# Kernel tuning notes

Hardware: AMD Instinct MI355X
Metric: run time of the kernel (lower is better)

## Reference

```python
import jax, jax.numpy as jnp
import numpy as np

B, LAT, HID = 256, 20, 128
G, BIN = 25000, 25       # original_dim, bin_size
C = 7                    # max_cp + 1 copy-number states
GB = G // BIN            # rho head output dim


def setup_inputs() -> dict:
    key = jax.random.key(0)
    ks = jax.random.split(key, 16)
    s = 0.01  # TruncatedNormal(stddev=0.01) init
    return {
        "z": jax.random.normal(ks[0], (B, LAT), jnp.float32),
        "w0": jax.random.normal(ks[1], (LAT, HID), jnp.float32) * s,
        "b0": jnp.zeros((HID,), jnp.float32),
        "g0": jnp.ones((HID,), jnp.float32),
        "be0": jnp.zeros((HID,), jnp.float32),
        "m0": jax.random.normal(ks[2], (HID,), jnp.float32) * 0.1,
        "v0": jax.random.uniform(ks[3], (HID,), jnp.float32, 0.5, 1.5),
        "w1": jax.random.normal(ks[4], (HID, HID), jnp.float32) * s,
        "b1": jnp.zeros((HID,), jnp.float32),
        "g1": jnp.ones((HID,), jnp.float32),
        "be1": jnp.zeros((HID,), jnp.float32),
        "m1": jax.random.normal(ks[5], (HID,), jnp.float32) * 0.1,
        "v1": jax.random.uniform(ks[6], (HID,), jnp.float32, 0.5, 1.5),
        "wr": jax.random.normal(ks[7], (HID, G), jnp.float32) * s,
        "br": jnp.zeros((G,), jnp.float32),
        "wd": jax.random.normal(ks[8], (HID, G), jnp.float32) * s,
        "bd": jnp.zeros((G,), jnp.float32),
        "wrho": jax.random.normal(ks[9], (C, HID, GB), jnp.float32) * s,
        "brho": jnp.zeros((C, GB), jnp.float32),
        "ws": jax.random.normal(ks[10], (G,), jnp.float32) * 0.05,
        "bs": jax.random.normal(ks[11], (G,), jnp.float32) * 0.05,
    }


def reference(z, w0, b0, g0, be0, m0, v0, w1, b1, g1, be1, m1, v1,
              wr, br, wd, bd, wrho, brho, ws, bs):
    BN_EPS = 1e-3
    EPS = 1e-20
    TEMP = 0.1

    def bn(x, gamma, beta, mean, var):
        # inference-mode BatchNormalization(momentum=0.01, epsilon=0.001)
        return (x - mean) * jax.lax.rsqrt(var + BN_EPS) * gamma + beta

    # FullyConnLayer x2: Dense -> BN -> ReLU
    x = jax.nn.relu(bn(z @ w0 + b0, g0, be0, m0, v0))
    x = jax.nn.relu(bn(x @ w1 + b1, g1, be1, m1, v1))

    theta = jnp.exp(x @ wr + br)        # [B, G]
    pi_drop = x @ wd + bd               # [B, G]

    # max_cp+1 rho Dense heads fused into a single batched GEMM -> [C, B, GB]
    rho = jnp.einsum('bh,cho->cbo', x, wrho) + brho[:, None, :]
    rho = jax.nn.softmax(rho, axis=0)   # softmax over copy-number states

    # GumbelSoftmaxSampling: stack(axis=1) -> [B, C, GB]
    rho_b = jnp.transpose(rho, (1, 0, 2))
    gene_rho = jnp.repeat(rho_b, BIN, axis=-1)        # [B, C, G]
    pi = jnp.transpose(gene_rho, (0, 2, 1))           # [B, G, C]

    u = jax.random.uniform(jax.random.key(42), pi.shape, jnp.float32)
    gnoise = -jnp.log(-jnp.log(u + EPS) + EPS)
    y = jax.nn.softmax((jnp.log(pi + EPS) + gnoise) / TEMP, axis=-1)
    y_hard = (y == jnp.max(y, axis=-1, keepdims=True)).astype(jnp.float32)
    y = jax.lax.stop_gradient(y_hard - y) + y         # straight-through

    # multiply by copy-number index matrix and reduce -> expected/sampled copy
    cvals = jnp.arange(C, dtype=jnp.float32)
    sample = jnp.sum(y * cvals, axis=-1)              # [B, G]

    # ScaleLayer: sigmoid(x * w + b)
    mu = jax.nn.sigmoid(sample * ws + bs)             # [B, G]
    return (mu, theta, pi_drop, sample, pi)
```

## Files before the change

### kernel.cpp

```cpp
#include <hip/hip_runtime.h>

#define B 256
#define LAT 20
#define HID 128
#define G 25000
#define GB 1000
#define NC 7

typedef __attribute__((ext_vector_type(8))) short short8;
typedef __attribute__((ext_vector_type(4))) float f32x4;

__device__ __forceinline__ unsigned short f2bf(float f) {
  unsigned int u = __float_as_uint(f);
  u += 0x7fffu + ((u >> 16) & 1u);
  return (unsigned short)(u >> 16);
}

__device__ __forceinline__ unsigned int threefry_xor(unsigned int idx) {
  unsigned int x0 = 0u;
  unsigned int x1 = idx + 42u;
#define TF_R(r) { x0 += x1; x1 = (x1 << r) | (x1 >> (32 - r)); x1 ^= x0; }
  TF_R(13) TF_R(15) TF_R(26) TF_R(6)
  x0 += 42u;          x1 += 0x1BD11BF1u;
  TF_R(17) TF_R(29) TF_R(16) TF_R(24)
  x0 += 0x1BD11BF0u;  x1 += 2u;
  TF_R(13) TF_R(15) TF_R(26) TF_R(6)
   x1 += 45u;
  TF_R(17) TF_R(29) TF_R(16) TF_R(24)
  x0 += 42u;          x1 += 0x1BD11BF4u;
  TF_R(13) TF_R(15) TF_R(26) TF_R(6)
  x0 += 0x1BD11BF0u;  x1 += 5u;
#undef TF_R
  return x0 ^ x1;
}

__global__ void k_mlp(const float* __restrict__ z,  const float* __restrict__ w0,
                      const float* __restrict__ b0, const float* __restrict__ g0,
                      const float* __restrict__ be0, const float* __restrict__ m0,
                      const float* __restrict__ v0,
                      const float* __restrict__ w1, const float* __restrict__ b1,
                      const float* __restrict__ g1, const float* __restrict__ be1,
                      const float* __restrict__ m1, const float* __restrict__ v1,
                      double* __restrict__ x64, unsigned short* __restrict__ x_bf) {
  __shared__ double xs[HID];
  const int b = blockIdx.x, h = threadIdx.x;
  double acc = (double)b0[h];
  for (int k = 0; k < LAT; ++k)
    acc += (double)z[b * LAT + k] * (double)w0[k * HID + h];
  double y = (acc - (double)m0[h]) * (1.0 / sqrt((double)v0[h] + 1e-3)) * (double)g0[h]
             + (double)be0[h];
  y = y > 0.0 ? y : 0.0;
  xs[h] = y;
  __syncthreads();
  double a1 = (double)b1[h];
  for (int k = 0; k < HID; ++k)
    a1 += xs[k] * (double)w1[k * HID + h];
  double y1 = (a1 - (double)m1[h]) * (1.0 / sqrt((double)v1[h] + 1e-3)) * (double)g1[h]
              + (double)be1[h];
  y1 = y1 > 0.0 ? y1 : 0.0;
  x64[h * B + b] = y1;
  x_bf[b * HID + h] = f2bf((float)y1);
}

__global__ void k_trans(const float* __restrict__ wr, const float* __restrict__ wd,
                        unsigned short* __restrict__ wrT, unsigned short* __restrict__ wdT) {
  __shared__ float t[64][65];
  const float* src = blockIdx.z ? wd : wr;
  unsigned short* dst = blockIdx.z ? wdT : wrT;
  const int g0 = blockIdx.x * 64, h0 = blockIdx.y * 64;
#pragma unroll
  for (int i = 0; i < 16; ++i) {
    int f = i * 256 + threadIdx.x;
    int hl = f >> 6, gl = f & 63;
    int g = g0 + gl;
    t[hl][gl] = (g < G) ? src[(h0 + hl) * G + g] : 0.f;
  }
  __syncthreads();
#pragma unroll
  for (int i = 0; i < 16; ++i) {
    int f = i * 256 + threadIdx.x;
    int gl = f >> 6, hl = f & 63;
    int g = g0 + gl;
    if (g < G) dst[(size_t)g * HID + h0 + hl] = f2bf(t[hl][gl]);
  }
}

__global__ __launch_bounds__(256) void k_rho(const double* __restrict__ x64,
                      const float* __restrict__ wrho, const float* __restrict__ brho,
                      float* __restrict__ pi32, float* __restrict__ lp32,
                      double* __restrict__ lp64) {
  __shared__ float wl[NC * HID * 4];
  const int o0 = blockIdx.x * 4, bB = blockIdx.y * 64;
  for (int i = threadIdx.x; i < NC * HID * 4; i += 256) {
    int ol = i & 3, rest = i >> 2;
    int c = rest >> 7, h = rest & 127;
    wl[i] = wrho[(c * HID + h) * GB + o0 + ol];
  }
  __syncthreads();
  const int lane = threadIdx.x & 63, ol = threadIdx.x >> 6;
  const int b = bB + lane, o = o0 + ol;
  double acc[NC];
#pragma unroll
  for (int c = 0; c < NC; ++c) acc[c] = (double)brho[c * GB + o];
  for (int h = 0; h < HID; ++h) {
    double xv = x64[h * B + b];
#pragma unroll
    for (int c = 0; c < NC; ++c)
      acc[c] += xv * (double)wl[(c * HID + h) * 4 + ol];
  }
  double m = acc[0];
#pragma unroll
  for (int c = 1; c < NC; ++c) m = fmax(m, acc[c]);
  double e[NC], s = 0.0;
#pragma unroll
  for (int c = 0; c < NC; ++c) { e[c] = exp(acc[c] - m); s += e[c]; }
  const size_t base = (size_t)o * (NC * B) + b;
#pragma unroll
  for (int c = 0; c < NC; ++c) {
    double pi = e[c] / s;
    double lp = log(pi + 1e-20);
    pi32[base + c * B] = (float)pi;
    lp32[base + c * B] = (float)lp;
    lp64[base + c * B] = lp;
  }
}

__global__ __launch_bounds__(256) void k_main(
    const unsigned short* __restrict__ x_bf,
    const unsigned short* __restrict__ wrT, const unsigned short* __restrict__ wdT,
    const float* __restrict__ br, const float* __restrict__ bd,
    const float* __restrict__ wsc, const float* __restrict__ bsc,
    const float* __restrict__ pi32, const float* __restrict__ lp32,
    const double* __restrict__ lp64, float* __restrict__ out) {
  const int tid = threadIdx.x;
  const int wv = tid >> 6, lane = tid & 63;
  const int n = lane & 15, quad = lane >> 4;
  const int gt = wv & 1;
  const int btbase = blockIdx.y * 8 + (wv >> 1) * 4;
  const int g = blockIdx.x * 32 + gt * 16 + n;
  const bool gvalid = g < G;
  const int gcl = gvalid ? g : G - 1;
  const float brv = br[gcl], bdv = bd[gcl], wsv = wsc[gcl], bsv = bsc[gcl];
  const int o = gcl / 25;
  const float*  lpb = lp32 + (size_t)o * (NC * B);
  const float*  pib = pi32 + (size_t)o * (NC * B);
  const double* lqb = lp64 + (size_t)o * (NC * B);

  short8 fr[4], fd[4];
  {
    const short8* p1 = (const short8*)(wrT + (size_t)gcl * HID + quad * 8);
    const short8* p2 = (const short8*)(wdT + (size_t)gcl * HID + quad * 8);
#pragma unroll
    for (int ks = 0; ks < 4; ++ks) { fr[ks] = p1[ks * 4]; fd[ks] = p2[ks * 4]; }
  }

  for (int bti = 0; bti < 4; ++bti) {
    const int bt = btbase + bti;
    const short8* xp = (const short8*)(x_bf + (size_t)(bt * 16 + n) * HID + quad * 8);
    f32x4 accr = {0.f, 0.f, 0.f, 0.f}, accd = {0.f, 0.f, 0.f, 0.f};
#pragma unroll
    for (int ks = 0; ks < 4; ++ks) {
      short8 fa = xp[ks * 4];
      accr = __builtin_amdgcn_mfma_f32_16x16x32_bf16(fa, fr[ks], accr, 0, 0, 0);
      accd = __builtin_amdgcn_mfma_f32_16x16x32_bf16(fa, fd[ks], accd, 0, 0, 0);
    }
#pragma unroll
    for (int i = 0; i < 4; ++i) {
      const int b = bt * 16 + quad * 4 + i;
      const float th = expf(accr[i] + brv);
      const float pd = accd[i] + bdv;
      float lpv[NC];
#pragma unroll
      for (int c = 0; c < NC; ++c) lpv[c] = lpb[c * B + b];
      unsigned int bits[NC];
      const unsigned int idx0 = (unsigned int)b * 175000u + (unsigned int)g * 7u;
      float best = -3.4e38f, sec = -3.4e38f; int arg = 0;
#pragma unroll
      for (int c = 0; c < NC; ++c) {
        unsigned int bb = threefry_xor(idx0 + (unsigned int)c);
        bits[c] = bb;
        float uf = __uint_as_float((bb >> 9) | 0x3f800000u) - 1.0f;
        float l1 = -logf(uf + 1e-20f);
        float gn = -__logf(l1 + 1e-20f);
        float mv = lpv[c] + gn;
        if (mv > best) { sec = best; best = mv; arg = c; }
        else if (mv > sec) sec = mv;
      }
      int s = arg;
      if (best - sec < 2e-3f) {
        double lv[NC], bestd = -1e300;
#pragma unroll
        for (int c = 0; c < NC; ++c) {
          float uf = __uint_as_float((bits[c] >> 9) | 0x3f800000u) - 1.0f;
          double gn = -log(-log((double)uf + 1e-20) + 1e-20);
          lv[c] = lqb[c * B + b] + gn;
          bestd = fmax(bestd, lv[c]);
        }
        s = 0;
#pragma unroll
        for (int c = 0; c < NC; ++c) if (lv[c] == bestd) s += c;
      }
      if (gvalid) {
        const float smp = (float)s;
        const float mu = 1.f / (1.f + expf(-(smp * wsv + bsv)));
        const size_t og = (size_t)b * G + g;
        out[og] = mu;
        out[6400000 + og] = th;
        out[12800000 + og] = pd;
        out[19200000 + og] = smp;
        const size_t pbo = 25600000 + og * 7;
#pragma unroll
        for (int c = 0; c < NC; ++c) out[pbo + c] = pib[c * B + b];
      }
    }
  }
}

extern "C" void kernel_launch(void* const* d_in, const int* in_sizes, int n_in,
                              void* d_out, int out_size, void* d_ws, size_t ws_size,
                              hipStream_t stream) {
  const float* z   = (const float*)d_in[0];
  const float* w0  = (const float*)d_in[1];
  const float* b0  = (const float*)d_in[2];
  const float* g0  = (const float*)d_in[3];
  const float* be0 = (const float*)d_in[4];
  const float* m0  = (const float*)d_in[5];
  const float* v0  = (const float*)d_in[6];
  const float* w1  = (const float*)d_in[7];
  const float* b1  = (const float*)d_in[8];
  const float* g1  = (const float*)d_in[9];
  const float* be1 = (const float*)d_in[10];
  const float* m1  = (const float*)d_in[11];
  const float* v1  = (const float*)d_in[12];
  const float* wr  = (const float*)d_in[13];
  const float* br  = (const float*)d_in[14];
  const float* wd  = (const float*)d_in[15];
  const float* bd  = (const float*)d_in[16];
  const float* wrho= (const float*)d_in[17];
  const float* brho= (const float*)d_in[18];
  const float* wsc = (const float*)d_in[19];
  const float* bsc = (const float*)d_in[20];

  char* ws = (char*)d_ws;
  unsigned short* x_bf = (unsigned short*)(ws);
  double* x64          = (double*)(ws + 65536);
  unsigned short* wrT  = (unsigned short*)(ws + 327680);
  unsigned short* wdT  = (unsigned short*)(ws + 6727680);
  float* pi32          = (float*)(ws + 13127680);
  float* lp32          = (float*)(ws + 20295680);
  double* lp64         = (double*)(ws + 27463680);
  float* out = (float*)d_out;

  k_mlp<<<dim3(256), dim3(128), 0, stream>>>(z, w0, b0, g0, be0, m0, v0,
                                             w1, b1, g1, be1, m1, v1, x64, x_bf);
  k_trans<<<dim3(391, 2, 2), dim3(256), 0, stream>>>(wr, wd, wrT, wdT);
  k_rho<<<dim3(250, 4), dim3(256), 0, stream>>>(x64, wrho, brho, pi32, lp32, lp64);
  k_main<<<dim3(782, 2), dim3(256), 0, stream>>>(x_bf, wrT, wdT, br, bd, wsc, bsc,
                                                 pi32, lp32, lp64, out);
}
```

Baseline: 550.7 us.

## Stage per-bin log-pi and pi in LDS, use fast math intrinsics

After: 522.3 us. 5.1% less time.

```diff
diff --git a/kernel.cpp b/kernel.cpp
--- a/kernel.cpp
+++ b/kernel.cpp
@@ -132,7 +132,22 @@
     const float* __restrict__ wsc, const float* __restrict__ bsc,
     const float* __restrict__ pi32, const float* __restrict__ lp32,
     const double* __restrict__ lp64, float* __restrict__ out) {
+  __shared__ float s_lp[3 * NC * 128];
+  __shared__ float s_pi[3 * NC * 128];
   const int tid = threadIdx.x;
+  const int o_base = (blockIdx.x * 32) / 25;
+  const int bB = blockIdx.y * 128;
+
+  for (int i = tid; i < 3 * NC * 128; i += 256) {
+    int ol = i / (NC * 128);
+    int r = i - ol * (NC * 128);
+    int c = r >> 7, bl = r & 127;
+    int oo = o_base + ol; if (oo > GB - 1) oo = GB - 1;
+    size_t src = (size_t)oo * (NC * B) + c * B + bB + bl;
+    s_lp[i] = lp32[src];
+    s_pi[i] = pi32[src];
+  }
+
   const int wv = tid >> 6, lane = tid & 63;
   const int n = lane & 15, quad = lane >> 4;
   const int gt = wv & 1;
@@ -142,8 +157,7 @@
   const int gcl = gvalid ? g : G - 1;
   const float brv = br[gcl], bdv = bd[gcl], wsv = wsc[gcl], bsv = bsc[gcl];
   const int o = gcl / 25;
-  const float*  lpb = lp32 + (size_t)o * (NC * B);
-  const float*  pib = pi32 + (size_t)o * (NC * B);
+  const int o_local = o - o_base;
   const double* lqb = lp64 + (size_t)o * (NC * B);
 
   short8 fr[4], fd[4];
@@ -153,6 +167,7 @@
 #pragma unroll
     for (int ks = 0; ks < 4; ++ks) { fr[ks] = p1[ks * 4]; fd[ks] = p2[ks * 4]; }
   }
+  __syncthreads();
 
   for (int bti = 0; bti < 4; ++bti) {
     const int bt = btbase + bti;
@@ -167,11 +182,10 @@
 #pragma unroll
     for (int i = 0; i < 4; ++i) {
       const int b = bt * 16 + quad * 4 + i;
-      const float th = expf(accr[i] + brv);
+      const int b_local = (wv >> 1) * 64 + bti * 16 + quad * 4 + i;
+      const float th = __expf(accr[i] + brv);
       const float pd = accd[i] + bdv;
-      float lpv[NC];
-#pragma unroll
-      for (int c = 0; c < NC; ++c) lpv[c] = lpb[c * B + b];
+      const float* lpp = s_lp + o_local * (NC * 128) + b_local;
       unsigned int bits[NC];
       const unsigned int idx0 = (unsigned int)b * 175000u + (unsigned int)g * 7u;
       float best = -3.4e38f, sec = -3.4e38f; int arg = 0;
@@ -180,14 +194,17 @@
         unsigned int bb = threefry_xor(idx0 + (unsigned int)c);
         bits[c] = bb;
         float uf = __uint_as_float((bb >> 9) | 0x3f800000u) - 1.0f;
-        float l1 = -logf(uf + 1e-20f);
-        float gn = -__logf(l1 + 1e-20f);
-        float mv = lpv[c] + gn;
+        float v1m = 1.0f - uf;
+        float ln_nat = -__logf(uf + 1e-20f);
+        float ln_ser = v1m * (1.0f + v1m * (0.5f + 0.33333334f * v1m));
+        float l1 = (v1m < 0.001953125f) ? ln_ser : ln_nat;
+        float gn = -__logf(l1);
+        float mv = lpp[c * 128] + gn;
         if (mv > best) { sec = best; best = mv; arg = c; }
         else if (mv > sec) sec = mv;
       }
       int s = arg;
-      if (best - sec < 2e-3f) {
+      if (best - sec < 3e-4f) {
         double lv[NC], bestd = -1e300;
 #pragma unroll
         for (int c = 0; c < NC; ++c) {
@@ -202,15 +219,16 @@
       }
       if (gvalid) {
         const float smp = (float)s;
-        const float mu = 1.f / (1.f + expf(-(smp * wsv + bsv)));
+        const float mu = __builtin_amdgcn_rcpf(1.f + __expf(-(smp * wsv + bsv)));
         const size_t og = (size_t)b * G + g;
         out[og] = mu;
         out[6400000 + og] = th;
         out[12800000 + og] = pd;
         out[19200000 + og] = smp;
+        const float* pip = s_pi + o_local * (NC * 128) + b_local;
         const size_t pbo = 25600000 + og * 7;
 #pragma unroll
-        for (int c = 0; c < NC; ++c) out[pbo + c] = pib[c * B + b];
+        for (int c = 0; c < NC; ++c) out[pbo + c] = pip[c * 128];
       }
     }
   }
```
